# Performance work log

Measured on AMD Instinct MI355X. Metric: run time of the kernel, lower is better.

Reference implementation:

```python
import jax, jax.numpy as jnp
import numpy as np

B, V, P, L, D = 8, 16, 128, 16, 128
PD = L * D  # patch_dim = patch_size * d_model = 2048


def _layernorm(x, g, b, eps=1e-5):
    mu = jnp.mean(x, axis=-1, keepdims=True)
    var = jnp.mean(jnp.square(x - mu), axis=-1, keepdims=True)
    return (x - mu) / jnp.sqrt(var + eps) * g + b


def setup_inputs() -> dict:
    key = jax.random.key(0)
    ks = jax.random.split(key, 24)
    x = jax.random.normal(ks[0], (B, V, P, L, D), jnp.float32)
    m = jax.random.randint(ks[1], (B, V, V), 0, 2) > 0
    var_mask = m & ~jnp.eye(V, dtype=bool)[None]  # keep self-attention unmasked

    def lin_w(k, fan_in, fan_out):
        return jax.random.normal(k, (fan_in, fan_out), jnp.float32) * (1.0 / np.sqrt(fan_in))

    inp = {"x": x, "var_mask": var_mask}
    # Attn_PatchLevel (attn1): query / shared kv / out projections
    inp["w_q1"] = lin_w(ks[2], PD, PD); inp["b_q1"] = jnp.zeros((PD,), jnp.float32)
    inp["w_kv1"] = lin_w(ks[3], PD, PD); inp["b_kv1"] = jnp.zeros((PD,), jnp.float32)
    inp["w_o1"] = lin_w(ks[4], PD, PD); inp["b_o1"] = jnp.zeros((PD,), jnp.float32)
    # Attn_VarLevel (attn2)
    inp["w_q2"] = lin_w(ks[5], PD, PD); inp["b_q2"] = jnp.zeros((PD,), jnp.float32)
    inp["w_kv2"] = lin_w(ks[6], PD, PD); inp["b_kv2"] = jnp.zeros((PD,), jnp.float32)
    inp["w_o2"] = lin_w(ks[7], PD, PD); inp["b_o2"] = jnp.zeros((PD,), jnp.float32)
    # LayerNorms
    inp["g1"] = jnp.ones((PD,), jnp.float32); inp["be1"] = jnp.zeros((PD,), jnp.float32)
    inp["g2"] = jnp.ones((PD,), jnp.float32); inp["be2"] = jnp.zeros((PD,), jnp.float32)
    inp["g3"] = jnp.ones((PD,), jnp.float32); inp["be3"] = jnp.zeros((PD,), jnp.float32)
    # FFN
    inp["w_l1"] = lin_w(ks[8], PD, 4 * PD); inp["b_l1"] = jnp.zeros((4 * PD,), jnp.float32)
    inp["w_l2"] = lin_w(ks[9], 4 * PD, PD); inp["b_l2"] = jnp.zeros((PD,), jnp.float32)
    return inp


def reference(x, var_mask,
              w_q1, b_q1, w_kv1, b_kv1, w_o1, b_o1,
              w_q2, b_q2, w_kv2, b_kv2, w_o2, b_o2,
              g1, be1, g2, be2, g3, be3,
              w_l1, b_l1, w_l2, b_l2):
    b, v, p, l, d = x.shape
    pd = l * d
    scale = 1.0 / np.sqrt(pd)
    x = x.reshape(b, v, p, pd)

    # ---- Attn_PatchLevel (mask=None -> no masking; keys and values share kv_projection) ----
    q = x @ w_q1 + b_q1
    kv = x @ w_kv1 + b_kv1  # keys == values in the original module
    scores = jnp.einsum('bvpd,bvsd->bvps', q, kv)  # [B,V,P,P]
    attn = jax.nn.softmax(scale * scores, axis=-1)  # dropout is identity at eval
    a1 = jnp.einsum('bvps,bvsd->bvpd', attn, kv) @ w_o1 + b_o1
    x = _layernorm(x + a1, g1, be1)

    # ---- Attn_VarLevel over variables, per patch ----
    x = x.transpose(0, 2, 1, 3)  # [B,P,V,PD]
    q = x @ w_q2 + b_q2
    kv = x @ w_kv2 + b_kv2
    scores = jnp.einsum('bpvd,bprd->bpvr', q, kv)  # [B,P,V,V]
    scores = jnp.where(var_mask[:, None, :, :], -jnp.inf, scores)
    attn = jax.nn.softmax(scale * scores, axis=-1)
    a2 = jnp.einsum('bpvr,bprd->bpvd', attn, kv) @ w_o2 + b_o2
    x = _layernorm(x + a2, g2, be2)

    # ---- FFN (torch nn.GELU default = exact erf) ----
    z = jax.nn.gelu(x @ w_l1 + b_l1, approximate=False)
    x = x + z @ w_l2 + b_l2

    x_out = _layernorm(x, g3, be3).transpose(0, 2, 1, 3)  # [B,V,P,PD]
    x_next = x_out.reshape(b, v, p // 2, 2 * l, d)
    return x_out, x_next
```

## Files before the change

### kernel.cpp

```cpp
#include <hip/hip_runtime.h>
#include <math.h>


using u16   = unsigned short;
using f32x4 = __attribute__((ext_vector_type(4))) float;
using bf16x8= __attribute__((ext_vector_type(8))) __bf16;
using u16x8 = __attribute__((ext_vector_type(8))) u16;
using u16x4 = __attribute__((ext_vector_type(4))) u16;

#define NROWS 16384
#define PD    2048

__device__ __forceinline__ float bf2f(u16 u) {
    unsigned v = ((unsigned)u) << 16;
    return __builtin_bit_cast(float, v);
}
__device__ __forceinline__ u16 f2bf(float f) {
    unsigned u = __builtin_bit_cast(unsigned, f);
    u += 0x7FFFu + ((u >> 16) & 1u);
    return (u16)(u >> 16);
}
__device__ __forceinline__ void gload_lds16(const void* g, void* l) {
    __builtin_amdgcn_global_load_lds((const __attribute__((address_space(1))) void*)g,
                                     (__attribute__((address_space(3))) void*)l, 16, 0, 0);
}

template<int GELU>
__global__ __launch_bounds__(512, 2)
void gemm256(const u16* __restrict__ A, int lda,
             const u16* __restrict__ B, int ldb,
             u16* __restrict__ C, int ldc,
             const float* __restrict__ bias, int K,
             int NT, int CM, int CN)
{
    __shared__ __align__(16) char smem[131072];

    const int tid  = threadIdx.x;
    const int wv   = tid >> 6;
    const int wm   = wv >> 2;
    const int wn   = wv & 3;
    const int lane = tid & 63;
    const int fr   = lane & 15;
    const int fks16= (lane >> 4) * 16;
    const int rmask= (fr & 7) << 4;
    const int kb0  = fks16 ^ rmask;
    const int kb1  = (64 + fks16) ^ rmask;

    const int xcd = blockIdx.x & 7;
    const int ii  = blockIdx.x >> 3;
    const int RY  = NT / CN;
    const int mt  = (xcd / RY) * CM + (ii / CN);
    const int nt  = (xcd % RY) * CN + (ii % CN);
    const int m0  = mt * 256;
    const int n0  = nt * 256;

    const int rsub = tid >> 3;
    const int cswE = (((tid & 7) * 16) ^ ((rsub & 7) << 4)) >> 1;
    const int waveByte = wv * 1024;

    auto stage = [&](const u16* mat, int ld, int row0, int k0, int regionByte) {
        const u16* g0 = mat + (size_t)(row0 + rsub) * ld + k0 + cswE;
        gload_lds16(g0,               smem + regionByte + waveByte);
        gload_lds16(g0 + (size_t)ld * 64, smem + regionByte + 8192 + waveByte);
    };

    const int aRowByte = (wm * 128 + fr) * 128;
    const int bRowByte = (wn * 64 + fr) * 128;

    const int KT = K >> 6;

    stage(A, lda, m0,       0, 0);
    stage(B, ldb, n0,       0, 32768);
    stage(A, lda, m0 + 128, 0, 16384);
    stage(B, ldb, n0 + 128, 0, 49152);
    stage(B, ldb, n0,      64, 98304);
    stage(A, lda, m0,      64, 65536);
    asm volatile("s_waitcnt vmcnt(4)" ::: "memory");
    __builtin_amdgcn_s_barrier();

    bf16x8 a[4][2], b0[2][2], b1[2][2];
    f32x4  acc[8][4] = {};

    for (int t = 0; t < KT; ++t) {
        const int Ab = (t & 1) ? 65536 : 0;
        const int Bb = Ab + 32768;
        const int Ob = Ab ^ 65536;
        const bool s1 = (t + 1 < KT), s2 = (t + 2 < KT);

        #pragma unroll
        for (int mi = 0; mi < 4; ++mi) {
            const int rb = Ab + aRowByte + mi * 2048;
            a[mi][0] = *(const bf16x8*)(smem + rb + kb0);
            a[mi][1] = *(const bf16x8*)(smem + rb + kb1);
        }
        #pragma unroll
        for (int nj = 0; nj < 2; ++nj) {
            const int rb = Bb + bRowByte + nj * 2048;
            b0[nj][0] = *(const bf16x8*)(smem + rb + kb0);
            b0[nj][1] = *(const bf16x8*)(smem + rb + kb1);
        }
        if (s1) stage(B, ldb, n0 + 128, (t + 1) << 6, Ob + 49152);
        __builtin_amdgcn_s_barrier();
        asm volatile("s_waitcnt lgkmcnt(0)" ::: "memory");
        __builtin_amdgcn_sched_barrier(0);
        __builtin_amdgcn_s_setprio(1);
        #pragma unroll
        for (int mi = 0; mi < 4; ++mi)
            #pragma unroll
            for (int nj = 0; nj < 2; ++nj) {
                acc[mi][nj] = __builtin_amdgcn_mfma_f32_16x16x32_bf16(a[mi][0], b0[nj][0], acc[mi][nj], 0, 0, 0);
                acc[mi][nj] = __builtin_amdgcn_mfma_f32_16x16x32_bf16(a[mi][1], b0[nj][1], acc[mi][nj], 0, 0, 0);
            }
        __builtin_amdgcn_s_setprio(0);
        __builtin_amdgcn_s_barrier();

        #pragma unroll
        for (int nj = 0; nj < 2; ++nj) {
            const int rb = Bb + bRowByte + 4096 + nj * 2048;
            b1[nj][0] = *(const bf16x8*)(smem + rb + kb0);
            b1[nj][1] = *(const bf16x8*)(smem + rb + kb1);
        }
        if (s1) stage(A, lda, m0 + 128, (t + 1) << 6, Ob + 16384);
        __builtin_amdgcn_s_barrier();
        asm volatile("s_waitcnt lgkmcnt(0)" ::: "memory");
        __builtin_amdgcn_sched_barrier(0);
        __builtin_amdgcn_s_setprio(1);
        #pragma unroll
        for (int mi = 0; mi < 4; ++mi)
            #pragma unroll
            for (int nj = 0; nj < 2; ++nj) {
                acc[mi][2 + nj] = __builtin_amdgcn_mfma_f32_16x16x32_bf16(a[mi][0], b1[nj][0], acc[mi][2 + nj], 0, 0, 0);
                acc[mi][2 + nj] = __builtin_amdgcn_mfma_f32_16x16x32_bf16(a[mi][1], b1[nj][1], acc[mi][2 + nj], 0, 0, 0);
            }
        __builtin_amdgcn_s_setprio(0);
        __builtin_amdgcn_s_barrier();

        #pragma unroll
        for (int mi = 0; mi < 4; ++mi) {
            const int rb = Ab + aRowByte + 8192 + mi * 2048;
            a[mi][0] = *(const bf16x8*)(smem + rb + kb0);
            a[mi][1] = *(const bf16x8*)(smem + rb + kb1);
        }
        if (s2) stage(B, ldb, n0, (t + 2) << 6, Bb);
        __builtin_amdgcn_s_barrier();
        asm volatile("s_waitcnt lgkmcnt(0)" ::: "memory");
        __builtin_amdgcn_sched_barrier(0);
        __builtin_amdgcn_s_setprio(1);
        #pragma unroll
        for (int mi = 0; mi < 4; ++mi)
            #pragma unroll
            for (int nj = 0; nj < 2; ++nj) {
                acc[4 + mi][nj] = __builtin_amdgcn_mfma_f32_16x16x32_bf16(a[mi][0], b0[nj][0], acc[4 + mi][nj], 0, 0, 0);
                acc[4 + mi][nj] = __builtin_amdgcn_mfma_f32_16x16x32_bf16(a[mi][1], b0[nj][1], acc[4 + mi][nj], 0, 0, 0);
            }
        __builtin_amdgcn_s_setprio(0);
        __builtin_amdgcn_s_barrier();

        if (s2) stage(A, lda, m0, (t + 2) << 6, Ab);
        __builtin_amdgcn_s_barrier();
        __builtin_amdgcn_s_setprio(1);
        #pragma unroll
        for (int mi = 0; mi < 4; ++mi)
            #pragma unroll
            for (int nj = 0; nj < 2; ++nj) {
                acc[4 + mi][2 + nj] = __builtin_amdgcn_mfma_f32_16x16x32_bf16(a[mi][0], b1[nj][0], acc[4 + mi][2 + nj], 0, 0, 0);
                acc[4 + mi][2 + nj] = __builtin_amdgcn_mfma_f32_16x16x32_bf16(a[mi][1], b1[nj][1], acc[4 + mi][2 + nj], 0, 0, 0);
            }
        __builtin_amdgcn_s_setprio(0);
        if (s2) { asm volatile("s_waitcnt vmcnt(4)" ::: "memory"); }
        else    { asm volatile("s_waitcnt vmcnt(0)" ::: "memory"); }
        __builtin_amdgcn_s_barrier();
    }

    const int colBase = n0 + wn * 64 + fr;
    const int rowBase = m0 + wm * 128 + (lane >> 4) * 4;
    #pragma unroll
    for (int nj = 0; nj < 4; ++nj) {
        const int col = colBase + nj * 16;
        const float bb = bias[col];
        #pragma unroll
        for (int mi = 0; mi < 8; ++mi) {
            #pragma unroll
            for (int j = 0; j < 4; ++j) {
                const int row = rowBase + mi * 16 + j;
                float v = acc[mi][nj][j] + bb;
                if constexpr (GELU) v = 0.5f * v * (1.f + erff(v * 0.70710678118f));
                C[(size_t)row * ldc + col] = f2bf(v);
            }
        }
    }
}

template<int OUTF32, int HASBIAS>
__global__ __launch_bounds__(256, 2)
void gemm_nt(const u16* __restrict__ A, long sAg, int lda,
             const u16* __restrict__ B, long sBg, int ldb,
             void* __restrict__ Cv, long sCg, int ldc,
             const float* __restrict__ bias, int K, float scale)
{
    __shared__ __align__(16) u16 lsA[128 * 32];
    __shared__ __align__(16) u16 lsB[128 * 32];

    const int tid  = threadIdx.x;
    const int w    = tid >> 6;
    const int lane = tid & 63;
    const int m0   = blockIdx.x * 128;
    const int n0   = blockIdx.y * 128;
    A += (long)blockIdx.z * sAg;
    B += (long)blockIdx.z * sBg;

    const int wr = w >> 1, wc = w & 1;
    f32x4 acc[4][4] = {};

    const int srow = lane >> 2;
    const int skc  = (lane & 3) * 8;
    const int rA0  = 32 * w + srow;
    const int rA1  = rA0 + 16;
    const size_t aoff0 = (size_t)(m0 + rA0) * lda + skc;
    const size_t aoff1 = (size_t)(m0 + rA1) * lda + skc;
    const size_t boff0 = (size_t)(n0 + rA0) * ldb + skc;
    const size_t boff1 = (size_t)(n0 + rA1) * ldb + skc;
    u16* lA0 = lsA + 1024 * w;
    u16* lA1 = lA0 + 512;
    u16* lB0 = lsB + 1024 * w;
    u16* lB1 = lB0 + 512;

    const int fr = lane & 15;
    const int fk = (lane >> 4) * 8;

    for (int k0 = 0; k0 < K; k0 += 32) {
        gload_lds16(A + aoff0 + k0, lA0);
        gload_lds16(A + aoff1 + k0, lA1);
        gload_lds16(B + boff0 + k0, lB0);
        gload_lds16(B + boff1 + k0, lB1);
        __syncthreads();

        bf16x8 af[4], bf[4];
        #pragma unroll
        for (int m = 0; m < 4; m++)
            af[m] = *(const bf16x8*)&lsA[(wr * 64 + m * 16 + fr) * 32 + fk];
        #pragma unroll
        for (int n = 0; n < 4; n++)
            bf[n] = *(const bf16x8*)&lsB[(wc * 64 + n * 16 + fr) * 32 + fk];
        #pragma unroll
        for (int m = 0; m < 4; m++)
            #pragma unroll
            for (int n = 0; n < 4; n++)
                acc[m][n] = __builtin_amdgcn_mfma_f32_16x16x32_bf16(af[m], bf[n], acc[m][n], 0, 0, 0);
        __syncthreads();
    }

    float* Cf = (float*)Cv;
    u16*   Cb = (u16*)Cv;
    const int crow0 = m0 + wr * 64 + (lane >> 4) * 4;
    const int ccol0 = n0 + wc * 64 + fr;
    const long cbase = (long)blockIdx.z * sCg;
    #pragma unroll
    for (int n = 0; n < 4; n++) {
        const int col = ccol0 + n * 16;
        float bb = 0.f;
        if constexpr (HASBIAS) bb = bias[col];
        #pragma unroll
        for (int m = 0; m < 4; m++) {
            #pragma unroll
            for (int j = 0; j < 4; j++) {
                const int row = crow0 + m * 16 + j;
                float v = acc[m][n][j] + bb;
                const long idx = cbase + (long)row * ldc + col;
                if constexpr (OUTF32) Cf[idx] = v * scale;
                else                  Cb[idx] = f2bf(v);
            }
        }
    }
}

__global__ __launch_bounds__(256)
void wtrans_kernel(const float* __restrict__ in, u16* __restrict__ out, int R, int C)
{
    __shared__ float tile[32][33];
    const int c0 = blockIdx.x * 32, r0 = blockIdx.y * 32;
    const int tx = threadIdx.x & 31, ty = threadIdx.x >> 5;
    #pragma unroll
    for (int i = ty; i < 32; i += 8)
        tile[i][tx] = in[(size_t)(r0 + i) * C + c0 + tx];
    __syncthreads();
    #pragma unroll
    for (int i = ty; i < 32; i += 8)
        out[(size_t)(c0 + i) * R + r0 + tx] = f2bf(tile[tx][i]);
}

__global__ __launch_bounds__(256)
void kvtrans_kernel(const u16* __restrict__ in, u16* __restrict__ out)
{
    __shared__ u16 tile[32][33];
    const int g = blockIdx.z;
    const int n0 = blockIdx.x * 32, m0 = blockIdx.y * 32;
    const int tx = threadIdx.x & 31, ty = threadIdx.x >> 5;
    #pragma unroll
    for (int i = ty; i < 32; i += 8)
        tile[i][tx] = in[(size_t)(g * 128 + m0 + i) * 2048 + n0 + tx];
    __syncthreads();
    #pragma unroll
    for (int i = ty; i < 32; i += 8)
        out[(size_t)g * 262144 + (size_t)(n0 + i) * 128 + m0 + tx] = tile[tx][i];
}

__global__ __launch_bounds__(256)
void cvt_f32_bf16(const float* __restrict__ in, u16* __restrict__ out)
{
    const long i = ((long)blockIdx.x * 256 + threadIdx.x) * 4;
    float4 v = *(const float4*)(in + i);
    u16x4 o;
    o[0] = f2bf(v.x); o[1] = f2bf(v.y); o[2] = f2bf(v.z); o[3] = f2bf(v.w);
    *(u16x4*)(out + i) = o;
}

template<int FINAL>
__global__ __launch_bounds__(256)
void ln_kernel(const float* __restrict__ resid, const u16* __restrict__ add,
               const float* __restrict__ gam, const float* __restrict__ bet,
               u16* __restrict__ xb, float* __restrict__ o1, float* __restrict__ o2)
{
    const long row = blockIdx.x;
    const int  t   = threadIdx.x;
    const long base = row * PD + t * 8;

    u16x8  av = *(const u16x8*)(add + base);
    float4 r0 = *(const float4*)(resid + base);
    float4 r1 = *(const float4*)(resid + base + 4);
    float y[8];
    y[0] = r0.x + bf2f(av[0]); y[1] = r0.y + bf2f(av[1]);
    y[2] = r0.z + bf2f(av[2]); y[3] = r0.w + bf2f(av[3]);
    y[4] = r1.x + bf2f(av[4]); y[5] = r1.y + bf2f(av[5]);
    y[6] = r1.z + bf2f(av[6]); y[7] = r1.w + bf2f(av[7]);

    float s1 = 0.f, s2 = 0.f;
    #pragma unroll
    for (int j = 0; j < 8; j++) { s1 += y[j]; s2 += y[j] * y[j]; }
    #pragma unroll
    for (int d = 1; d < 64; d <<= 1) { s1 += __shfl_xor(s1, d); s2 += __shfl_xor(s2, d); }
    __shared__ float red[8];
    const int w = t >> 6;
    if ((t & 63) == 0) { red[w] = s1; red[4 + w] = s2; }
    __syncthreads();
    s1 = red[0] + red[1] + red[2] + red[3];
    s2 = red[4] + red[5] + red[6] + red[7];
    const float mean = s1 * (1.f / PD);
    const float var  = s2 * (1.f / PD) - mean * mean;
    const float rstd = rsqrtf(var + 1e-5f);

    float4 g0 = *(const float4*)(gam + t * 8);
    float4 g1 = *(const float4*)(gam + t * 8 + 4);
    float4 b0 = *(const float4*)(bet + t * 8);
    float4 b1 = *(const float4*)(bet + t * 8 + 4);
    float gv[8] = {g0.x, g0.y, g0.z, g0.w, g1.x, g1.y, g1.z, g1.w};
    float bv[8] = {b0.x, b0.y, b0.z, b0.w, b1.x, b1.y, b1.z, b1.w};

    float o[8];
    #pragma unroll
    for (int j = 0; j < 8; j++) o[j] = (y[j] - mean) * rstd * gv[j] + bv[j];

    if constexpr (FINAL) {
        float4 p0 = {o[0], o[1], o[2], o[3]}, p1 = {o[4], o[5], o[6], o[7]};
        *(float4*)(o1 + base) = p0; *(float4*)(o1 + base + 4) = p1;
        *(float4*)(o2 + base) = p0; *(float4*)(o2 + base + 4) = p1;
    } else {
        u16x8 ob;
        #pragma unroll
        for (int j = 0; j < 8; j++) ob[j] = f2bf(o[j]);
        *(u16x8*)(xb + base) = ob;
        float4 p0 = {o[0], o[1], o[2], o[3]}, p1 = {o[4], o[5], o[6], o[7]};
        *(float4*)(o1 + base) = p0; *(float4*)(o1 + base + 4) = p1;
    }
}

__global__ __launch_bounds__(256)
void softmax128_kernel(const float* __restrict__ S, u16* __restrict__ P)
{
    const int row  = blockIdx.x * 4 + (threadIdx.x >> 6);
    const int lane = threadIdx.x & 63;
    const float2 v = *(const float2*)(S + (size_t)row * 128 + lane * 2);
    float mx = fmaxf(v.x, v.y);
    #pragma unroll
    for (int d = 1; d < 64; d <<= 1) mx = fmaxf(mx, __shfl_xor(mx, d));
    const float e0 = __expf(v.x - mx), e1 = __expf(v.y - mx);
    float sm = e0 + e1;
    #pragma unroll
    for (int d = 1; d < 64; d <<= 1) sm += __shfl_xor(sm, d);
    const float inv = 1.f / sm;
    unsigned o = (unsigned)f2bf(e0 * inv) | ((unsigned)f2bf(e1 * inv) << 16);
    *(unsigned*)(P + (size_t)row * 128 + lane * 2) = o;
}

__global__ void detect_mask_kernel(const unsigned char* __restrict__ m, int* __restrict__ flag)
{
    __shared__ int s;
    if (threadIdx.x == 0) s = 0;
    __syncthreads();
    int acc = 0;
    for (int i = threadIdx.x; i < 2048; i += 256)
        if (i & 3) acc |= m[i];
    if (acc) atomicOr(&s, 1);
    __syncthreads();
    if (threadIdx.x == 0) *flag = s;
}

__global__ __launch_bounds__(64)
void attn2_kernel(u16* __restrict__ Q, const u16* __restrict__ KV,
                  const void* __restrict__ mask, const int* __restrict__ mflag,
                  float scale)
{
    const int g = blockIdx.x;
    const int b = g >> 7, p = g & 127;
    const int lane = threadIdx.x;

    const size_t groupbase = ((size_t)(b * 16) * 128 + p) * PD;
    const size_t vstride   = (size_t)128 * PD;

    const int am   = lane & 15;
    const int koff = (lane >> 4) * 8;
    const u16* qp = Q  + groupbase + (size_t)am * vstride + koff;
    const u16* kp = KV + groupbase + (size_t)am * vstride + koff;

    f32x4 acc = {0.f, 0.f, 0.f, 0.f};
    for (int k0 = 0; k0 < PD; k0 += 32) {
        bf16x8 a  = *(const bf16x8*)(qp + k0);
        bf16x8 bb = *(const bf16x8*)(kp + k0);
        acc = __builtin_amdgcn_mfma_f32_16x16x32_bf16(a, bb, acc, 0, 0, 0);
    }

    const int vk = lane & 15;
    const int hi = lane >> 4;
    const int mf = *mflag;
    __shared__ float PL[16][16];
    float pv[4];
    #pragma unroll
    for (int j = 0; j < 4; j++) {
        const int vq = hi * 4 + j;
        float s = acc[j] * scale;
        const int midx = b * 256 + vq * 16 + vk;
        int msk;
        if (mf) msk = ((const unsigned char*)mask)[midx];
        else    msk = ((const int*)mask)[midx];
        if (msk) s = -1e30f;
        pv[j] = s;
    }
    #pragma unroll
    for (int j = 0; j < 4; j++) {
        float mx = pv[j];
        #pragma unroll
        for (int d = 1; d < 16; d <<= 1) mx = fmaxf(mx, __shfl_xor(mx, d));
        const float e = __expf(pv[j] - mx);
        float sm = e;
        #pragma unroll
        for (int d = 1; d < 16; d <<= 1) sm += __shfl_xor(sm, d);
        pv[j] = e / sm;
    }
    #pragma unroll
    for (int j = 0; j < 4; j++) PL[hi * 4 + j][vk] = pv[j];
    __syncthreads();

    const u16* kvr[16];
    #pragma unroll
    for (int v = 0; v < 16; v++) kvr[v] = KV + groupbase + (size_t)v * vstride;

    for (int vqt = 0; vqt < 16; vqt += 4) {
        float pr[4][16];
        #pragma unroll
        for (int q = 0; q < 4; q++)
            #pragma unroll
            for (int k = 0; k < 16; k++) pr[q][k] = PL[vqt + q][k];
        u16* o0 = Q + groupbase + (size_t)(vqt + 0) * vstride;
        u16* o1 = Q + groupbase + (size_t)(vqt + 1) * vstride;
        u16* o2 = Q + groupbase + (size_t)(vqt + 2) * vstride;
        u16* o3 = Q + groupbase + (size_t)(vqt + 3) * vstride;
        for (int n0 = 0; n0 < PD; n0 += 64) {
            const int n = n0 + lane;
            float a0 = 0.f, a1 = 0.f, a2 = 0.f, a3 = 0.f;
            #pragma unroll
            for (int k = 0; k < 16; k++) {
                const float kvv = bf2f(kvr[k][n]);
                a0 += pr[0][k] * kvv; a1 += pr[1][k] * kvv;
                a2 += pr[2][k] * kvv; a3 += pr[3][k] * kvv;
            }
            o0[n] = f2bf(a0); o1[n] = f2bf(a1); o2[n] = f2bf(a2); o3[n] = f2bf(a3);
        }
    }
}

extern "C" void kernel_launch(void* const* d_in, const int* in_sizes, int n_in,
                              void* d_out, int out_size, void* d_ws, size_t ws_size,
                              hipStream_t stream)
{
    const float* x0    = (const float*)d_in[0];
    const void*  vmask = d_in[1];
    const float* b_q1  = (const float*)d_in[3];
    const float* b_kv1 = (const float*)d_in[5];
    const float* b_o1  = (const float*)d_in[7];
    const float* b_q2  = (const float*)d_in[9];
    const float* b_kv2 = (const float*)d_in[11];
    const float* b_o2  = (const float*)d_in[13];
    const float* w_q1  = (const float*)d_in[2];
    const float* w_kv1 = (const float*)d_in[4];
    const float* w_o1  = (const float*)d_in[6];
    const float* w_q2  = (const float*)d_in[8];
    const float* w_kv2 = (const float*)d_in[10];
    const float* w_o2  = (const float*)d_in[12];
    const float* g1 = (const float*)d_in[14]; const float* be1 = (const float*)d_in[15];
    const float* g2 = (const float*)d_in[16]; const float* be2 = (const float*)d_in[17];
    const float* g3 = (const float*)d_in[18]; const float* be3 = (const float*)d_in[19];
    const float* w_l1 = (const float*)d_in[20]; const float* b_l1 = (const float*)d_in[21];
    const float* w_l2 = (const float*)d_in[22]; const float* b_l2 = (const float*)d_in[23];

    char* ws = (char*)d_ws;
    size_t off = 0;
    auto alloc = [&](size_t bytes) { size_t o = off; off += (bytes + 255) & ~(size_t)255; return o; };
    const size_t oWQ1  = alloc(8388608),  oWKV1 = alloc(8388608),  oWO1 = alloc(8388608);
    const size_t oWQ2  = alloc(8388608),  oWKV2 = alloc(8388608),  oWO2 = alloc(8388608);
    const size_t oWL1  = alloc(33554432), oWL2  = alloc(33554432);
    const size_t oXB   = alloc(67108864);
    const size_t oQ    = alloc(67108864);
    const size_t oKV   = alloc(67108864);
    const size_t oKVT  = alloc(67108864);
    const size_t oR    = alloc(134217728);
    const size_t oS    = alloc(8388608);
    const size_t oP1   = alloc(4194304);
    const size_t oFLAG = alloc(256);
    if (ws_size < off) return;

    u16* WQ1T = (u16*)(ws + oWQ1);  u16* WKV1T = (u16*)(ws + oWKV1); u16* WO1T = (u16*)(ws + oWO1);
    u16* WQ2T = (u16*)(ws + oWQ2);  u16* WKV2T = (u16*)(ws + oWKV2); u16* WO2T = (u16*)(ws + oWO2);
    u16* WL1T = (u16*)(ws + oWL1);  u16* WL2T  = (u16*)(ws + oWL2);
    u16* XB   = (u16*)(ws + oXB);   u16* Q     = (u16*)(ws + oQ);
    u16* KV   = (u16*)(ws + oKV);   u16* KVT   = (u16*)(ws + oKVT);
    float* R  = (float*)(ws + oR);  float* S   = (float*)(ws + oS);
    u16* P1   = (u16*)(ws + oP1);   int* FLAG  = (int*)(ws + oFLAG);
    u16* H    = Q;
    u16* F    = KVT;

    const float scale = 0.02209708691f;
    float* out0 = (float*)d_out;
    float* out1 = out0 + (size_t)NROWS * PD;

    detect_mask_kernel<<<1, 256, 0, stream>>>((const unsigned char*)vmask, FLAG);

    wtrans_kernel<<<dim3(64, 64), 256, 0, stream>>>(w_q1,  WQ1T,  2048, 2048);
    wtrans_kernel<<<dim3(64, 64), 256, 0, stream>>>(w_kv1, WKV1T, 2048, 2048);
    wtrans_kernel<<<dim3(64, 64), 256, 0, stream>>>(w_o1,  WO1T,  2048, 2048);
    wtrans_kernel<<<dim3(64, 64), 256, 0, stream>>>(w_q2,  WQ2T,  2048, 2048);
    wtrans_kernel<<<dim3(64, 64), 256, 0, stream>>>(w_kv2, WKV2T, 2048, 2048);
    wtrans_kernel<<<dim3(64, 64), 256, 0, stream>>>(w_o2,  WO2T,  2048, 2048);
    wtrans_kernel<<<dim3(256, 64), 256, 0, stream>>>(w_l1, WL1T, 2048, 8192);
    wtrans_kernel<<<dim3(64, 256), 256, 0, stream>>>(w_l2, WL2T, 8192, 2048);

    cvt_f32_bf16<<<32768, 256, 0, stream>>>(x0, XB);


    gemm256<0><<<512, 512, 0, stream>>>(XB, 2048, WQ1T,  2048, Q,  2048, b_q1,  2048, 8, 16, 4);
    gemm256<0><<<512, 512, 0, stream>>>(XB, 2048, WKV1T, 2048, KV, 2048, b_kv1, 2048, 8, 16, 4);
    kvtrans_kernel<<<dim3(64, 4, 128), 256, 0, stream>>>(KV, KVT);
    gemm_nt<1,0><<<dim3(1,1,128), 256, 0, stream>>>(Q, 262144, 2048, KV, 262144, 2048, S, 16384, 128, nullptr, 2048, scale);
    softmax128_kernel<<<4096, 256, 0, stream>>>(S, P1);
    gemm_nt<0,0><<<dim3(1,16,128), 256, 0, stream>>>(P1, 16384, 128, KVT, 262144, 128, Q, 262144, 2048, nullptr, 128, 1.f);
    gemm256<0><<<512, 512, 0, stream>>>(Q, 2048, WO1T, 2048, KV, 2048, b_o1, 2048, 8, 16, 4);
    ln_kernel<0><<<NROWS, 256, 0, stream>>>(x0, KV, g1, be1, XB, R, nullptr);

    gemm256<0><<<512, 512, 0, stream>>>(XB, 2048, WQ2T,  2048, Q,  2048, b_q2,  2048, 8, 16, 4);
    gemm256<0><<<512, 512, 0, stream>>>(XB, 2048, WKV2T, 2048, KV, 2048, b_kv2, 2048, 8, 16, 4);
    attn2_kernel<<<1024, 64, 0, stream>>>(Q, KV, vmask, FLAG, scale);
    gemm256<0><<<512, 512, 0, stream>>>(Q, 2048, WO2T, 2048, KV, 2048, b_o2, 2048, 8, 16, 4);
    ln_kernel<0><<<NROWS, 256, 0, stream>>>(R, KV, g2, be2, XB, R, nullptr);

    for (int c = 0; c < 2; c++) {
        const size_t rows = (size_t)c * 8192;
        gemm256<1><<<1024, 512, 0, stream>>>(XB + rows * 2048, 2048, WL1T, 2048, H, 8192, b_l1, 2048, 32, 32, 4);
        gemm256<0><<<256,  512, 0, stream>>>(H, 8192, WL2T, 8192, F + rows * 2048, 2048, b_l2, 8192, 8, 32, 1);
    }
    ln_kernel<1><<<NROWS, 256, 0, stream>>>(R, F, g3, be3, nullptr, out0, out1);
}
```

Baseline: 2.567 ms.

## Trim GEMM barriers, stage epilogue through LDS, retune tile swizzle and split FFN1

Removes the per-phase s_barrier, lgkmcnt wait and sched_barrier that sat before each MFMA block, relying on the compiler to insert LDS waits, which cuts synchronization overhead. Changes the epilogue to write bf16 results into LDS and then store full 16-byte coalesced rows to global memory instead of scattered 2-byte stores. Also retunes the XCD tile grouping parameters (CM/CN) for the 2048x2048 GEMMs and splits the FFN1 GEMM into two half-width launches. Dropping barriers risks LDS races between the asynchronous global-to-LDS staging and reads by other waves.

Measured after the change: 2.431 ms. -5.3%, faster.

```diff
diff --git a/kernel.cpp b/kernel.cpp
--- a/kernel.cpp
+++ b/kernel.cpp
@@ -10,6 +10,7 @@
 
 #define NROWS 16384
 #define PD    2048
+#define MEMBAR asm volatile("" ::: "memory")
 
 __device__ __forceinline__ float bf2f(u16 u) {
     unsigned v = ((unsigned)u) << 16;
@@ -23,6 +24,9 @@
 __device__ __forceinline__ void gload_lds16(const void* g, void* l) {
     __builtin_amdgcn_global_load_lds((const __attribute__((address_space(1))) void*)g,
                                      (__attribute__((address_space(3))) void*)l, 16, 0, 0);
+}
+__device__ __forceinline__ void block_barrier() {
+    MEMBAR; __builtin_amdgcn_s_barrier(); MEMBAR;
 }
 
 template<int GELU>
@@ -60,7 +64,7 @@
 
     auto stage = [&](const u16* mat, int ld, int row0, int k0, int regionByte) {
         const u16* g0 = mat + (size_t)(row0 + rsub) * ld + k0 + cswE;
-        gload_lds16(g0,               smem + regionByte + waveByte);
+        gload_lds16(g0,                   smem + regionByte + waveByte);
         gload_lds16(g0 + (size_t)ld * 64, smem + regionByte + 8192 + waveByte);
     };
 
@@ -76,7 +80,7 @@
     stage(B, ldb, n0,      64, 98304);
     stage(A, lda, m0,      64, 65536);
     asm volatile("s_waitcnt vmcnt(4)" ::: "memory");
-    __builtin_amdgcn_s_barrier();
+    block_barrier();
 
     bf16x8 a[4][2], b0[2][2], b1[2][2];
     f32x4  acc[8][4] = {};
@@ -100,9 +104,6 @@
             b0[nj][1] = *(const bf16x8*)(smem + rb + kb1);
         }
         if (s1) stage(B, ldb, n0 + 128, (t + 1) << 6, Ob + 49152);
-        __builtin_amdgcn_s_barrier();
-        asm volatile("s_waitcnt lgkmcnt(0)" ::: "memory");
-        __builtin_amdgcn_sched_barrier(0);
         __builtin_amdgcn_s_setprio(1);
         #pragma unroll
         for (int mi = 0; mi < 4; ++mi)
@@ -112,7 +113,7 @@
                 acc[mi][nj] = __builtin_amdgcn_mfma_f32_16x16x32_bf16(a[mi][1], b0[nj][1], acc[mi][nj], 0, 0, 0);
             }
         __builtin_amdgcn_s_setprio(0);
-        __builtin_amdgcn_s_barrier();
+        block_barrier();
 
         #pragma unroll
         for (int nj = 0; nj < 2; ++nj) {
@@ -121,9 +122,6 @@
             b1[nj][1] = *(const bf16x8*)(smem + rb + kb1);
         }
         if (s1) stage(A, lda, m0 + 128, (t + 1) << 6, Ob + 16384);
-        __builtin_amdgcn_s_barrier();
-        asm volatile("s_waitcnt lgkmcnt(0)" ::: "memory");
-        __builtin_amdgcn_sched_barrier(0);
         __builtin_amdgcn_s_setprio(1);
         #pragma unroll
         for (int mi = 0; mi < 4; ++mi)
@@ -133,7 +131,7 @@
                 acc[mi][2 + nj] = __builtin_amdgcn_mfma_f32_16x16x32_bf16(a[mi][1], b1[nj][1], acc[mi][2 + nj], 0, 0, 0);
             }
         __builtin_amdgcn_s_setprio(0);
-        __builtin_amdgcn_s_barrier();
+        block_barrier();
 
         #pragma unroll
         for (int mi = 0; mi < 4; ++mi) {
@@ -142,9 +140,6 @@
             a[mi][1] = *(const bf16x8*)(smem + rb + kb1);
         }
         if (s2) stage(B, ldb, n0, (t + 2) << 6, Bb);
-        __builtin_amdgcn_s_barrier();
-        asm volatile("s_waitcnt lgkmcnt(0)" ::: "memory");
-        __builtin_amdgcn_sched_barrier(0);
         __builtin_amdgcn_s_setprio(1);
         #pragma unroll
         for (int mi = 0; mi < 4; ++mi)
@@ -154,10 +149,9 @@
                 acc[4 + mi][nj] = __builtin_amdgcn_mfma_f32_16x16x32_bf16(a[mi][1], b0[nj][1], acc[4 + mi][nj], 0, 0, 0);
             }
         __builtin_amdgcn_s_setprio(0);
-        __builtin_amdgcn_s_barrier();
+        block_barrier();
 
         if (s2) stage(A, lda, m0, (t + 2) << 6, Ab);
-        __builtin_amdgcn_s_barrier();
         __builtin_amdgcn_s_setprio(1);
         #pragma unroll
         for (int mi = 0; mi < 4; ++mi)
@@ -169,25 +163,33 @@
         __builtin_amdgcn_s_setprio(0);
         if (s2) { asm volatile("s_waitcnt vmcnt(4)" ::: "memory"); }
         else    { asm volatile("s_waitcnt vmcnt(0)" ::: "memory"); }
-        __builtin_amdgcn_s_barrier();
-    }
-
-    const int colBase = n0 + wn * 64 + fr;
-    const int rowBase = m0 + wm * 128 + (lane >> 4) * 4;
+        block_barrier();
+    }
+
+    u16* lsu = (u16*)smem;
+    const int lcol = wn * 64 + fr;
+    const int lrow = wm * 128 + (lane >> 4) * 4;
     #pragma unroll
     for (int nj = 0; nj < 4; ++nj) {
-        const int col = colBase + nj * 16;
-        const float bb = bias[col];
+        const float bb = bias[n0 + lcol + nj * 16];
         #pragma unroll
         for (int mi = 0; mi < 8; ++mi) {
             #pragma unroll
             for (int j = 0; j < 4; ++j) {
-                const int row = rowBase + mi * 16 + j;
                 float v = acc[mi][nj][j] + bb;
                 if constexpr (GELU) v = 0.5f * v * (1.f + erff(v * 0.70710678118f));
-                C[(size_t)row * ldc + col] = f2bf(v);
-            }
-        }
+                lsu[(lrow + mi * 16 + j) * 256 + lcol + nj * 16] = f2bf(v);
+            }
+        }
+    }
+    block_barrier();
+    const int hp = tid & 31;
+    const int r0 = tid >> 5;
+    #pragma unroll
+    for (int ps = 0; ps < 16; ++ps) {
+        const int r = ps * 16 + r0;
+        u16x8 v = *(const u16x8*)&lsu[r * 256 + hp * 8];
+        *(u16x8*)&C[(size_t)(m0 + r) * ldc + n0 + hp * 8] = v;
     }
 }
 
@@ -494,18 +496,12 @@
 {
     const float* x0    = (const float*)d_in[0];
     const void*  vmask = d_in[1];
-    const float* b_q1  = (const float*)d_in[3];
-    const float* b_kv1 = (const float*)d_in[5];
-    const float* b_o1  = (const float*)d_in[7];
-    const float* b_q2  = (const float*)d_in[9];
-    const float* b_kv2 = (const float*)d_in[11];
-    const float* b_o2  = (const float*)d_in[13];
-    const float* w_q1  = (const float*)d_in[2];
-    const float* w_kv1 = (const float*)d_in[4];
-    const float* w_o1  = (const float*)d_in[6];
-    const float* w_q2  = (const float*)d_in[8];
-    const float* w_kv2 = (const float*)d_in[10];
-    const float* w_o2  = (const float*)d_in[12];
+    const float* w_q1  = (const float*)d_in[2];  const float* b_q1  = (const float*)d_in[3];
+    const float* w_kv1 = (const float*)d_in[4];  const float* b_kv1 = (const float*)d_in[5];
+    const float* w_o1  = (const float*)d_in[6];  const float* b_o1  = (const float*)d_in[7];
+    const float* w_q2  = (const float*)d_in[8];  const float* b_q2  = (const float*)d_in[9];
+    const float* w_kv2 = (const float*)d_in[10]; const float* b_kv2 = (const float*)d_in[11];
+    const float* w_o2  = (const float*)d_in[12]; const float* b_o2  = (const float*)d_in[13];
     const float* g1 = (const float*)d_in[14]; const float* be1 = (const float*)d_in[15];
     const float* g2 = (const float*)d_in[16]; const float* be2 = (const float*)d_in[17];
     const float* g3 = (const float*)d_in[18]; const float* be3 = (const float*)d_in[19];
@@ -556,25 +552,30 @@
     cvt_f32_bf16<<<32768, 256, 0, stream>>>(x0, XB);
 
 
-    gemm256<0><<<512, 512, 0, stream>>>(XB, 2048, WQ1T,  2048, Q,  2048, b_q1,  2048, 8, 16, 4);
-    gemm256<0><<<512, 512, 0, stream>>>(XB, 2048, WKV1T, 2048, KV, 2048, b_kv1, 2048, 8, 16, 4);
+    gemm256<0><<<512, 512, 0, stream>>>(XB, 2048, WQ1T,  2048, Q,  2048, b_q1,  2048, 8, 32, 2);
+    gemm256<0><<<512, 512, 0, stream>>>(XB, 2048, WKV1T, 2048, KV, 2048, b_kv1, 2048, 8, 32, 2);
     kvtrans_kernel<<<dim3(64, 4, 128), 256, 0, stream>>>(KV, KVT);
     gemm_nt<1,0><<<dim3(1,1,128), 256, 0, stream>>>(Q, 262144, 2048, KV, 262144, 2048, S, 16384, 128, nullptr, 2048, scale);
     softmax128_kernel<<<4096, 256, 0, stream>>>(S, P1);
     gemm_nt<0,0><<<dim3(1,16,128), 256, 0, stream>>>(P1, 16384, 128, KVT, 262144, 128, Q, 262144, 2048, nullptr, 128, 1.f);
-    gemm256<0><<<512, 512, 0, stream>>>(Q, 2048, WO1T, 2048, KV, 2048, b_o1, 2048, 8, 16, 4);
+    gemm256<0><<<512, 512, 0, stream>>>(Q, 2048, WO1T, 2048, KV, 2048, b_o1, 2048, 8, 32, 2);
     ln_kernel<0><<<NROWS, 256, 0, stream>>>(x0, KV, g1, be1, XB, R, nullptr);
 
-    gemm256<0><<<512, 512, 0, stream>>>(XB, 2048, WQ2T,  2048, Q,  2048, b_q2,  2048, 8, 16, 4);
-    gemm256<0><<<512, 512, 0, stream>>>(XB, 2048, WKV2T, 2048, KV, 2048, b_kv2, 2048, 8, 16, 4);
+    gemm256<0><<<512, 512, 0, stream>>>(XB, 2048, WQ2T,  2048, Q,  2048, b_q2,  2048, 8, 32, 2);
+    gemm256<0><<<512, 512, 0, stream>>>(XB, 2048, WKV2T, 2048, KV, 2048, b_kv2, 2048, 8, 32, 2);
     attn2_kernel<<<1024, 64, 0, stream>>>(Q, KV, vmask, FLAG, scale);
-    gemm256<0><<<512, 512, 0, stream>>>(Q, 2048, WO2T, 2048, KV, 2048, b_o2, 2048, 8, 16, 4);
+    gemm256<0><<<512, 512, 0, stream>>>(Q, 2048, WO2T, 2048, KV, 2048, b_o2, 2048, 8, 32, 2);
     ln_kernel<0><<<NROWS, 256, 0, stream>>>(R, KV, g2, be2, XB, R, nullptr);
 
     for (int c = 0; c < 2; c++) {
         const size_t rows = (size_t)c * 8192;
-        gemm256<1><<<1024, 512, 0, stream>>>(XB + rows * 2048, 2048, WL1T, 2048, H, 8192, b_l1, 2048, 32, 32, 4);
-        gemm256<0><<<256,  512, 0, stream>>>(H, 8192, WL2T, 8192, F + rows * 2048, 2048, b_l2, 8192, 8, 32, 1);
+        for (int h = 0; h < 2; h++) {
+            gemm256<1><<<512, 512, 0, stream>>>(XB + rows * 2048, 2048,
+                                                WL1T + (size_t)h * 4096 * 2048, 2048,
+                                                H + h * 4096, 8192,
+                                                b_l1 + h * 4096, 2048, 16, 32, 2);
+        }
+        gemm256<0><<<256, 512, 0, stream>>>(H, 8192, WL2T, 8192, F + rows * 2048, 2048, b_l2, 8192, 8, 32, 1);
     }
     ln_kernel<1><<<NROWS, 256, 0, stream>>>(R, F, g3, be3, nullptr, out0, out1);
 }
```
